# Kernel tuning notes

Measured on AMD Instinct MI355X. Metric: run time of the kernel, lower is better.

Reference implementation:

```python
import jax, jax.numpy as jnp
import numpy as np
from jax import lax

EPS = 1e-5
DIM_1D, DIM_2D, CH, L, B = 788, 210, 64, 384, 1
DILATIONS = (1, 2, 4, 2, 1)


def inorm(x, gamma, beta, axes):
    # InstanceNorm: normalize over spatial axes per (batch, channel), affine params per channel
    mu = jnp.mean(x, axis=axes, keepdims=True)
    var = jnp.mean(jnp.square(x - mu), axis=axes, keepdims=True)
    xn = (x - mu) * lax.rsqrt(var + EPS)
    shape = [1] * x.ndim
    shape[1] = x.shape[1]
    return xn * gamma.reshape(shape) + beta.reshape(shape)


def inorm_noaffine(x, axes):
    mu = jnp.mean(x, axis=axes, keepdims=True)
    var = jnp.mean(jnp.square(x - mu), axis=axes, keepdims=True)
    return (x - mu) * lax.rsqrt(var + EPS)


def conv3x3(x, w, b, d):
    y = lax.conv_general_dilated(x, w, window_strides=(1, 1),
                                 padding=[(d, d), (d, d)], rhs_dilation=(d, d),
                                 dimension_numbers=('NCHW', 'OIHW', 'NCHW'))
    return y + b.reshape(1, -1, 1, 1)


def setup_inputs() -> dict:
    key = jax.random.key(0)
    ks = jax.random.split(key, 16)
    s = 0.02
    inp = {
        'x_1d': jax.random.normal(ks[0], (B, DIM_1D, L), jnp.float32),
        'x_2d': jax.random.normal(ks[1], (B, DIM_2D, L, L), jnp.float32),
        'W1': jax.random.normal(ks[2], (CH, 2 * DIM_1D), jnp.float32) * s,
        'g1': jnp.ones((CH,), jnp.float32), 'b1': jnp.zeros((CH,), jnp.float32),
        'W2': jax.random.normal(ks[3], (CH, DIM_2D), jnp.float32) * s,
        'g2': jnp.ones((CH,), jnp.float32), 'b2': jnp.zeros((CH,), jnp.float32),
        'W3': jax.random.normal(ks[4], (CH, 2 * CH), jnp.float32) * s,
        'g3': jnp.ones((CH,), jnp.float32), 'b3': jnp.zeros((CH,), jnp.float32),
        'res_w': jax.random.normal(ks[5], (5, 2, CH, CH, 3, 3), jnp.float32) * s,
        'res_b': jnp.zeros((5, 2, CH), jnp.float32),
        'res_g': jnp.ones((5, 2, CH), jnp.float32),
        'res_beta': jnp.zeros((5, 2, CH), jnp.float32),
    }
    return inp


def reference(x_1d, x_2d, W1, g1, b1, W2, g2, b2, W3, g3, b3,
              res_w, res_b, res_g, res_beta):
    # pre-norms (no affine)
    x1 = inorm_noaffine(x_1d, axes=(2,))            # [B, D1, L]
    x2 = inorm_noaffine(x_2d, axes=(2, 3))          # [B, D2, L, L]

    # pair_conv1: 1x1 conv on concat(row-expand, col-expand) of x1.
    # Mathematically: W1a @ x1 broadcast over j  +  W1b @ x1 broadcast over i.
    W1a, W1b = W1[:, :DIM_1D], W1[:, DIM_1D:]
    row = jnp.einsum('cd,bdl->bcl', W1a, x1)        # [B, C, L] (row term, index i)
    col = jnp.einsum('cd,bdl->bcl', W1b, x1)        # [B, C, L] (col term, index j)
    pair1 = row[:, :, :, None] + col[:, :, None, :]  # [B, C, L, L]
    pair1 = jax.nn.leaky_relu(inorm(pair1, g1, b1, axes=(2, 3)), 0.01)

    # pair_conv2: 1x1 conv on x2
    pair2 = jnp.einsum('cd,bdij->bcij', W2, x2)
    pair2 = jax.nn.leaky_relu(inorm(pair2, g2, b2, axes=(2, 3)), 0.01)

    # pair_conv3: 1x1 conv on concat([pair1, pair2]) -> split weight, sum
    W3a, W3b = W3[:, :CH], W3[:, CH:]
    pair = jnp.einsum('cd,bdij->bcij', W3a, pair1) + jnp.einsum('cd,bdij->bcij', W3b, pair2)
    x = jax.nn.leaky_relu(inorm(pair, g3, b3, axes=(2, 3)), 0.01)

    # ResNet: 5 blocks, each (conv-IN-lrelu) x2 + residual, dropout=0
    for layer in range(5):
        d = DILATIONS[layer]
        res = x
        for k in range(2):
            x = conv3x3(x, res_w[layer, k], res_b[layer, k], d)
            x = jax.nn.leaky_relu(inorm(x, res_g[layer, k], res_beta[layer, k], axes=(2, 3)), 0.01)
        x = x + res
    return x
```

## Files before the change

kernel.cpp:

```cpp
#include <hip/hip_runtime.h>
#include <hip/hip_bf16.h>

typedef __attribute__((ext_vector_type(8)))  short short8;
typedef __attribute__((ext_vector_type(16))) float floatx16;
typedef unsigned short ushort;

constexpr int SL  = 384;
constexpr int N2  = SL * SL;
constexpr int CH  = 64;
constexpr int D1  = 788;
constexpr int D2  = 210;
constexpr int KG2 = 14;
constexpr float EPSF = 1e-5f;

constexpr int TX = 32, TY = 8;
constexpr int NBLK = (SL / TX) * (SL / TY);


__device__ __forceinline__ float lrelu(float v){ return v >= 0.f ? v : 0.01f * v; }
__device__ __forceinline__ ushort f2b(float f){
  __hip_bfloat16 h = __float2bfloat16(f); return *(ushort*)&h;
}
__device__ __forceinline__ float b2f(ushort u){
  __hip_bfloat16 h = *(__hip_bfloat16*)&u; return __bfloat162float(h);
}

__device__ __forceinline__ float wred(float v){
  #pragma unroll
  for (int o = 32; o; o >>= 1) v += __shfl_down(v, o, 64);
  return v;
}

__global__ void stats_k(const float* __restrict__ x, int n, float* __restrict__ part){
  const int c = blockIdx.y, s = blockIdx.x, S = gridDim.x;
  const int chunk = (n + S - 1) / S;
  const int st = s * chunk, en = min(n, st + chunk);
  const float* p = x + (size_t)c * n;
  float sm = 0.f, ss = 0.f;
  for (int i = st + threadIdx.x; i < en; i += blockDim.x){
    float v = p[i]; sm += v; ss += v * v;
  }
  sm = wred(sm); ss = wred(ss);
  __shared__ float aux[8];
  const int wid = threadIdx.x >> 6, lane = threadIdx.x & 63;
  if (lane == 0){ aux[wid] = sm; aux[4 + wid] = ss; }
  __syncthreads();
  if (threadIdx.x == 0){
    part[((size_t)c * S + s) * 2]     = aux[0] + aux[1] + aux[2] + aux[3];
    part[((size_t)c * S + s) * 2 + 1] = aux[4] + aux[5] + aux[6] + aux[7];
  }
}

__global__ void stats_final_k(const float* __restrict__ part, int C, int S, float ninv,
                              float* __restrict__ mean, float* __restrict__ rstd){
  const int c = blockIdx.x * 64 + (threadIdx.x >> 4);
  const int t = threadIdx.x & 15;
  if (c >= C) return;
  float sm = 0.f, ss = 0.f;
  for (int s = t; s < S; s += 16){
    sm += part[((size_t)c * S + s) * 2];
    ss += part[((size_t)c * S + s) * 2 + 1];
  }
  #pragma unroll
  for (int o = 8; o; o >>= 1){ sm += __shfl_down(sm, o, 16); ss += __shfl_down(ss, o, 16); }
  if (t == 0){
    const float m = sm * ninv;
    mean[c] = m;
    rstd[c] = rsqrtf(ss * ninv - m * m + EPSF);
  }
}

__global__ void statsaffine_k(const float* __restrict__ part, int S, float ninv,
                              const float* __restrict__ g, const float* __restrict__ be,
                              int goff, float* __restrict__ ao, float* __restrict__ bo){
  const int c = threadIdx.x >> 4;
  const int t = threadIdx.x & 15;
  float sm = 0.f, ss = 0.f;
  for (int s = t; s < S; s += 16){
    sm += part[((size_t)c * S + s) * 2];
    ss += part[((size_t)c * S + s) * 2 + 1];
  }
  #pragma unroll
  for (int o = 8; o; o >>= 1){ sm += __shfl_down(sm, o, 16); ss += __shfl_down(ss, o, 16); }
  if (t == 0){
    const float m = sm * ninv;
    const float r = rsqrtf(ss * ninv - m * m + EPSF);
    const float a = r * g[goff + c];
    ao[c] = a;
    bo[c] = be[goff + c] - m * a;
  }
}

__global__ void rowcol_k(const float* __restrict__ x1d, const float* __restrict__ W1,
                         const float* __restrict__ r1, float* __restrict__ rcP){
  const int idx = blockIdx.x * 256 + threadIdx.x;
  const int chunk = blockIdx.y;
  const int half = idx / (CH * SL);
  const int rem  = idx % (CH * SL);
  const int c = rem / SL, l = rem % SL;
  const int d0 = chunk * 197, d1 = min(D1, d0 + 197);
  const float* wp = W1 + (size_t)c * (2 * D1) + (size_t)half * D1;
  float acc = 0.f;
  for (int d = d0; d < d1; ++d)
    acc += wp[d] * (x1d[(size_t)d * SL + l] * r1[d]);
  rcP[(size_t)chunk * (2 * CH * SL) + idx] = acc;
}

__global__ void rowcol_stats_k(const float* __restrict__ rcP,
                               float* __restrict__ m1, float* __restrict__ rs1){
  const int c = blockIdx.x;
  float sr = 0, ssr = 0, sc = 0, ssc = 0;
  for (int i = threadIdx.x; i < SL; i += blockDim.x){
    float r = 0, q = 0;
    #pragma unroll
    for (int k = 0; k < 4; ++k){
      r += rcP[(size_t)k * (2*CH*SL) + c * SL + i];
      q += rcP[(size_t)k * (2*CH*SL) + CH*SL + c * SL + i];
    }
    sr += r; ssr += r * r; sc += q; ssc += q * q;
  }
  sr = wred(sr); ssr = wred(ssr); sc = wred(sc); ssc = wred(ssc);
  __shared__ float aux[16];
  const int wid = threadIdx.x >> 6, lane = threadIdx.x & 63;
  if (lane == 0){ aux[wid] = sr; aux[4+wid] = ssr; aux[8+wid] = sc; aux[12+wid] = ssc; }
  __syncthreads();
  if (threadIdx.x == 0){
    float a = 0, b = 0, d = 0, e = 0;
    for (int i = 0; i < 4; ++i){ a += aux[i]; b += aux[4+i]; d += aux[8+i]; e += aux[12+i]; }
    const float mr = a / SL, mc = d / SL;
    const float vr = b / SL - mr * mr, vc = e / SL - mc * mc;
    m1[c]  = mr + mc;
    rs1[c] = rsqrtf(vr + vc + EPSF);
  }
}

__global__ void rowcolT_k(const float* __restrict__ rcP,
                          const float* __restrict__ m1, const float* __restrict__ rs1,
                          const float* __restrict__ g1, const float* __restrict__ b1,
                          float* __restrict__ rowT, float* __restrict__ colT){
  const int i = blockIdx.x * 256 + threadIdx.x;
  const int l = i >> 6, c = i & 63;
  float r = 0, q = 0;
  #pragma unroll
  for (int k = 0; k < 4; ++k){
    r += rcP[(size_t)k * (2*CH*SL) + c * SL + l];
    q += rcP[(size_t)k * (2*CH*SL) + CH*SL + c * SL + l];
  }
  const float a  = rs1[c] * g1[c];
  const float bb = b1[c] - m1[c] * a;
  rowT[i] = r * a + bb;
  colT[i] = q * a;
}

__global__ __launch_bounds__(256) void pair1n_k(const float* __restrict__ rowT,
                                                const float* __restrict__ colT,
                                                ushort* __restrict__ out){
  const size_t q = ((size_t)blockIdx.x * 256 + threadIdx.x) * 16;
  const int R = (int)(q >> 4);
  const int x = R % SL;
  const int t = R / SL;
  const int kc = t & 3, y = t >> 2;
  const int c0 = kc * 16;
  const float4* rp = (const float4*)&rowT[y * 64 + c0];
  const float4* cp = (const float4*)&colT[x * 64 + c0];
  ushort o[16];
  #pragma unroll
  for (int k = 0; k < 4; ++k){
    float4 r = rp[k], cl = cp[k];
    o[4*k]   = f2b(lrelu(r.x + cl.x));
    o[4*k+1] = f2b(lrelu(r.y + cl.y));
    o[4*k+2] = f2b(lrelu(r.z + cl.z));
    o[4*k+3] = f2b(lrelu(r.w + cl.w));
  }
  *(short8*)&out[q]     = *(short8*)&o[0];
  *(short8*)&out[q + 8] = *(short8*)&o[8];
}

__global__ __launch_bounds__(256) void x2cvt_k(const float* __restrict__ x2,
                                               ushort* __restrict__ x2b,
                                               float* __restrict__ part){
  const int g  = blockIdx.y;
  const int p  = blockIdx.x * 256 + threadIdx.x;
  const int tid = threadIdx.x;
  float v[16];
  #pragma unroll
  for (int i = 0; i < 16; ++i){
    const int d = g * 16 + i;
    v[i] = (d < D2) ? x2[(size_t)d * N2 + p] : 0.f;
  }
  ushort o[16];
  #pragma unroll
  for (int i = 0; i < 16; ++i) o[i] = f2b(v[i]);
  ushort* dp = &x2b[((size_t)g * N2 + p) * 16];
  *(short8*)&dp[0] = *(short8*)&o[0];
  *(short8*)&dp[8] = *(short8*)&o[8];
  __shared__ float aux[4][16][2];
  const int wid = tid >> 6, lane = tid & 63;
  #pragma unroll
  for (int i = 0; i < 16; ++i){
    float a = wred(v[i]), b = wred(v[i] * v[i]);
    if (lane == 0){ aux[wid][i][0] = a; aux[wid][i][1] = b; }
  }
  __syncthreads();
  if (tid < 16){
    const int d = g * 16 + tid;
    if (d < D2){
      float a = aux[0][tid][0] + aux[1][tid][0] + aux[2][tid][0] + aux[3][tid][0];
      float b = aux[0][tid][1] + aux[1][tid][1] + aux[2][tid][1] + aux[3][tid][1];
      part[((size_t)d * gridDim.x + blockIdx.x) * 2]     = a;
      part[((size_t)d * gridDim.x + blockIdx.x) * 2 + 1] = b;
    }
  }
}

__global__ void w2b_k(const float* __restrict__ W2, const float* __restrict__ r2,
                      ushort* __restrict__ w2b){
  const int i = blockIdx.x * 256 + threadIdx.x;
  const int j    = i & 7;
  const int oc   = (i >> 3) & 63;
  const int half = (i >> 9) & 1;
  const int kc   = i >> 10;
  const int d    = kc * 16 + half * 8 + j;
  w2b[i] = (d < D2) ? f2b(W2[(size_t)oc * D2 + d] * r2[d]) : (ushort)0;
}

__global__ __launch_bounds__(256) void pair2m_k(const ushort* __restrict__ x2b,
                                                const ushort* __restrict__ w2b,
                                                ushort* __restrict__ out,
                                                float* __restrict__ part){
  __shared__ __align__(16) unsigned char ldsraw[256 * 144 + 4 * CH * 2 * 4];
  const int tid = threadIdx.x, lane = tid & 63, wid = tid >> 6;
  const int ln = lane & 31, half = lane >> 5;
  const int px0 = blockIdx.x * 256;
  floatx16 acc[2][2];
  #pragma unroll
  for (int mt = 0; mt < 2; ++mt)
    #pragma unroll
    for (int nt = 0; nt < 2; ++nt)
      #pragma unroll
      for (int r = 0; r < 16; ++r) acc[mt][nt][r] = 0.f;

  const int p0w = px0 + wid * 64 + ln;
  #pragma unroll
  for (int kc = 0; kc < KG2; ++kc){
    const ushort* ab = w2b + ((size_t)(kc * 2 + half)) * 512;
    short8 a0 = *(const short8*)&ab[ln * 8];
    short8 a1 = *(const short8*)&ab[256 + ln * 8];
    short8 b0 = *(const short8*)&x2b[((size_t)kc * N2 + p0w) * 16 + half * 8];
    short8 b1 = *(const short8*)&x2b[((size_t)kc * N2 + p0w + 32) * 16 + half * 8];
    acc[0][0] = __builtin_amdgcn_mfma_f32_32x32x16_bf16(a0, b0, acc[0][0], 0, 0, 0);
    acc[1][0] = __builtin_amdgcn_mfma_f32_32x32x16_bf16(a1, b0, acc[1][0], 0, 0, 0);
    acc[0][1] = __builtin_amdgcn_mfma_f32_32x32x16_bf16(a0, b1, acc[0][1], 0, 0, 0);
    acc[1][1] = __builtin_amdgcn_mfma_f32_32x32x16_bf16(a1, b1, acc[1][1], 0, 0, 0);
  }

  ushort* tb = (ushort*)ldsraw;
  float*  sc = (float*)(ldsraw + 256 * 144);
  #pragma unroll
  for (int mt = 0; mt < 2; ++mt)
    #pragma unroll
    for (int nt = 0; nt < 2; ++nt){
      const int pxl = (2*wid + nt) * 32 + ln;
      #pragma unroll
      for (int rq = 0; rq < 4; ++rq){
        const int oc0 = mt*32 + 8*rq + 4*half;
        #pragma unroll
        for (int k = 0; k < 2; ++k){
          const int r = rq*4 + k*2;
          unsigned pk = (unsigned)f2b(acc[mt][nt][r]) | ((unsigned)f2b(acc[mt][nt][r+1]) << 16);
          *(unsigned*)&tb[pxl * 72 + oc0 + k*2] = pk;
        }
      }
    }
  #pragma unroll
  for (int mt = 0; mt < 2; ++mt)
    #pragma unroll
    for (int rq = 0; rq < 4; ++rq)
      #pragma unroll
      for (int t = 0; t < 4; ++t){
        const int r = rq*4 + t;
        float v  = acc[mt][0][r] + acc[mt][1][r];
        float v2 = acc[mt][0][r]*acc[mt][0][r] + acc[mt][1][r]*acc[mt][1][r];
        #pragma unroll
        for (int o = 1; o < 32; o <<= 1){ v += __shfl_xor(v, o, 64); v2 += __shfl_xor(v2, o, 64); }
        if (ln == 0){
          const int oc = mt*32 + 8*rq + 4*half + t;
          sc[(wid*CH + oc)*2] = v; sc[(wid*CH + oc)*2 + 1] = v2;
        }
      }
  __syncthreads();
  {
    const int px = lane & 31, h2 = lane >> 5;
    #pragma unroll
    for (int nt = 0; nt < 2; ++nt){
      const int rr = 2*wid + nt;
      const int p = px0 + rr*32 + px;
      const int y = p / SL, x = p - y * SL;
      #pragma unroll
      for (int h = 0; h < 2; ++h){
        const int kc = h2*2 + h;
        const ushort* sp = &tb[(rr*32 + px) * 72 + kc*16];
        ushort* dp = &out[((size_t)((y*4 + kc) * SL) + x) * 16];
        *(short8*)&dp[0] = *(const short8*)&sp[0];
        *(short8*)&dp[8] = *(const short8*)&sp[8];
      }
    }
  }
  if (tid < CH){
    float sm = 0.f, ss = 0.f;
    #pragma unroll
    for (int w = 0; w < 4; ++w){ sm += sc[(w*CH + tid)*2]; ss += sc[(w*CH + tid)*2 + 1]; }
    part[((size_t)tid * NBLK + blockIdx.x) * 2]     = sm;
    part[((size_t)tid * NBLK + blockIdx.x) * 2 + 1] = ss;
  }
}

__global__ __launch_bounds__(256) void norm_nhwc_k(ushort* __restrict__ x,
                                                   const float* __restrict__ a,
                                                   const float* __restrict__ b){
  const size_t q = ((size_t)blockIdx.x * 256 + threadIdx.x) * 16;
  const int R = (int)(q >> 4);
  const int c0 = ((R / SL) & 3) * 16;
  short8 v0 = *(short8*)&x[q], v1 = *(short8*)&x[q + 8];
  ushort o[16];
  #pragma unroll
  for (int k = 0; k < 8; ++k){
    o[k]   = f2b(lrelu(b2f((ushort)v0[k]) * a[c0+k]   + b[c0+k]));
    o[k+8] = f2b(lrelu(b2f((ushort)v1[k]) * a[c0+8+k] + b[c0+8+k]));
  }
  *(short8*)&x[q]     = *(short8*)&o[0];
  *(short8*)&x[q + 8] = *(short8*)&o[8];
}

__global__ void w3b_k(const float* __restrict__ W3, ushort* __restrict__ w3b){
  const int i = blockIdx.x * 256 + threadIdx.x;
  const int j    = i & 7;
  const int oc   = (i >> 3) & 63;
  const int half = (i >> 9) & 1;
  const int kc   = i >> 10;
  const int e    = kc * 16 + half * 8 + j;
  w3b[i] = f2b(W3[oc * (2 * CH) + e]);
}

__global__ __launch_bounds__(256) void mixm_k(const ushort* __restrict__ A,
                                              const ushort* __restrict__ Bv,
                                              const ushort* __restrict__ w3b,
                                              ushort* __restrict__ out,
                                              float* __restrict__ part){
  __shared__ __align__(16) unsigned char ldsraw[256 * 144 + 4 * CH * 2 * 4];
  const int tid = threadIdx.x, lane = tid & 63, wid = tid >> 6;
  const int ln = lane & 31, half = lane >> 5;
  const int px0 = blockIdx.x * 256;
  floatx16 acc[2][2];
  #pragma unroll
  for (int mt = 0; mt < 2; ++mt)
    #pragma unroll
    for (int nt = 0; nt < 2; ++nt)
      #pragma unroll
      for (int r = 0; r < 16; ++r) acc[mt][nt][r] = 0.f;

  const int p0w = px0 + wid * 64 + ln;
  const int p1w = p0w + 32;
  const int y0 = p0w / SL, x0 = p0w - y0 * SL;
  const int y1 = p1w / SL, x1 = p1w - y1 * SL;
  #pragma unroll
  for (int kc = 0; kc < 8; ++kc){
    const ushort* src = (kc < 4) ? A : Bv;
    const int kcm = kc & 3;
    const ushort* ab = w3b + ((size_t)(kc * 2 + half)) * 512;
    short8 a0 = *(const short8*)&ab[ln * 8];
    short8 a1 = *(const short8*)&ab[256 + ln * 8];
    const size_t r0 = ((size_t)((y0 * 4 + kcm) * SL) + x0) * 16 + half * 8;
    const size_t r1 = ((size_t)((y1 * 4 + kcm) * SL) + x1) * 16 + half * 8;
    short8 b0 = *(const short8*)&src[r0];
    short8 b1 = *(const short8*)&src[r1];
    acc[0][0] = __builtin_amdgcn_mfma_f32_32x32x16_bf16(a0, b0, acc[0][0], 0, 0, 0);
    acc[1][0] = __builtin_amdgcn_mfma_f32_32x32x16_bf16(a1, b0, acc[1][0], 0, 0, 0);
    acc[0][1] = __builtin_amdgcn_mfma_f32_32x32x16_bf16(a0, b1, acc[0][1], 0, 0, 0);
    acc[1][1] = __builtin_amdgcn_mfma_f32_32x32x16_bf16(a1, b1, acc[1][1], 0, 0, 0);
  }

  ushort* tb = (ushort*)ldsraw;
  float*  sc = (float*)(ldsraw + 256 * 144);
  #pragma unroll
  for (int mt = 0; mt < 2; ++mt)
    #pragma unroll
    for (int nt = 0; nt < 2; ++nt){
      const int pxl = (2*wid + nt) * 32 + ln;
      #pragma unroll
      for (int rq = 0; rq < 4; ++rq){
        const int oc0 = mt*32 + 8*rq + 4*half;
        #pragma unroll
        for (int k = 0; k < 2; ++k){
          const int r = rq*4 + k*2;
          unsigned pk = (unsigned)f2b(acc[mt][nt][r]) | ((unsigned)f2b(acc[mt][nt][r+1]) << 16);
          *(unsigned*)&tb[pxl * 72 + oc0 + k*2] = pk;
        }
      }
    }
  #pragma unroll
  for (int mt = 0; mt < 2; ++mt)
    #pragma unroll
    for (int rq = 0; rq < 4; ++rq)
      #pragma unroll
      for (int t = 0; t < 4; ++t){
        const int r = rq*4 + t;
        float v  = acc[mt][0][r] + acc[mt][1][r];
        float v2 = acc[mt][0][r]*acc[mt][0][r] + acc[mt][1][r]*acc[mt][1][r];
        #pragma unroll
        for (int o = 1; o < 32; o <<= 1){ v += __shfl_xor(v, o, 64); v2 += __shfl_xor(v2, o, 64); }
        if (ln == 0){
          const int oc = mt*32 + 8*rq + 4*half + t;
          sc[(wid*CH + oc)*2] = v; sc[(wid*CH + oc)*2 + 1] = v2;
        }
      }
  __syncthreads();
  {
    const int px = lane & 31, h2 = lane >> 5;
    #pragma unroll
    for (int nt = 0; nt < 2; ++nt){
      const int rr = 2*wid + nt;
      const int p = px0 + rr*32 + px;
      const int y = p / SL, x = p - y * SL;
      #pragma unroll
      for (int h = 0; h < 2; ++h){
        const int kc = h2*2 + h;
        const ushort* sp = &tb[(rr*32 + px) * 72 + kc*16];
        ushort* dp = &out[((size_t)((y*4 + kc) * SL) + x) * 16];
        *(short8*)&dp[0] = *(const short8*)&sp[0];
        *(short8*)&dp[8] = *(const short8*)&sp[8];
      }
    }
  }
  if (tid < CH){
    float sm = 0.f, ss = 0.f;
    #pragma unroll
    for (int w = 0; w < 4; ++w){ sm += sc[(w*CH + tid)*2]; ss += sc[(w*CH + tid)*2 + 1]; }
    part[((size_t)tid * NBLK + blockIdx.x) * 2]     = sm;
    part[((size_t)tid * NBLK + blockIdx.x) * 2 + 1] = ss;
  }
}

__global__ __launch_bounds__(256) void norm_res_k(const ushort* __restrict__ src,
                                                  const float* __restrict__ a,
                                                  const float* __restrict__ b,
                                                  float* __restrict__ X,
                                                  ushort* __restrict__ Xb,
                                                  int doRes){
  __shared__ float tf[64 * 68];
  const int tid = threadIdx.x;
  const int p0 = blockIdx.x * 64;
  const int y0 = p0 / SL, x0 = p0 - y0 * SL;
  const int pxl = tid >> 2, kc = tid & 3, c0 = kc * 16;
  {
    const ushort* sp = &src[((size_t)((y0*4 + kc) * SL) + x0 + pxl) * 16];
    short8 v0 = *(const short8*)&sp[0], v1 = *(const short8*)&sp[8];
    #pragma unroll
    for (int k = 0; k < 8; ++k){
      tf[(c0+k)*68 + pxl]   = lrelu(b2f((ushort)v0[k]) * a[c0+k]   + b[c0+k]);
      tf[(c0+8+k)*68 + pxl] = lrelu(b2f((ushort)v1[k]) * a[c0+8+k] + b[c0+8+k]);
    }
  }
  __syncthreads();
  {
    const int c = tid >> 2, part = tid & 3;
    const size_t gb = (size_t)c * N2 + p0 + part * 16;
    float w[16];
    #pragma unroll
    for (int k = 0; k < 16; ++k) w[k] = tf[c*68 + part*16 + k];
    if (doRes){
      #pragma unroll
      for (int k = 0; k < 16; ++k) w[k] += X[gb + k];
      #pragma unroll
      for (int k = 0; k < 16; ++k) tf[c*68 + part*16 + k] = w[k];
    }
    #pragma unroll
    for (int k = 0; k < 16; ++k) X[gb + k] = w[k];
  }
  if (Xb){
    __syncthreads();
    ushort o[16];
    #pragma unroll
    for (int k = 0; k < 16; ++k) o[k] = f2b(tf[(c0+k)*68 + pxl]);
    ushort* xp = &Xb[((size_t)((y0*4 + kc) * SL) + x0 + pxl) * 16];
    *(short8*)&xp[0] = *(short8*)&o[0];
    *(short8*)&xp[8] = *(short8*)&o[8];
  }
}

__global__ void wt_k(const float* __restrict__ w, ushort* __restrict__ wt){
  const int i = blockIdx.x * 256 + threadIdx.x;
  const int j    = i & 7;
  const int oc   = (i >> 3) & 63;
  const int half = (i >> 9) & 1;
  const int kc   = (i >> 10) & 3;
  const int tap  = (i / 4096) % 9;
  const int cv   = i / 36864;
  const int ic   = kc * 16 + half * 8 + j;
  wt[i] = f2b(w[((size_t)(cv * CH + oc) * CH + ic) * 9 + tap]);
}

template<int DIL, bool FUSE>
__global__ __launch_bounds__(256, 3) void convd_k(const ushort* __restrict__ in,
                                                  const ushort* __restrict__ wg,
                                                  const float* __restrict__ na,
                                                  const float* __restrict__ nb,
                                                  ushort* __restrict__ out,
                                                  float* __restrict__ part){
  constexpr int TH = TY + 2 * DIL;
  constexpr int TW = TX + 2 * DIL;
  constexpr int PHASES = (DIL >= 2) ? 2 : 1;
  constexpr int KCP = 4 / PHASES;
  constexpr int STAGE_B = KCP * TH * TW * 32;
  constexpr int EPI_B = 256 * 144 + 4 * CH * 2 * 4;
  constexpr int LDS_B = STAGE_B > EPI_B ? STAGE_B : EPI_B;
  __shared__ __align__(16) unsigned char ldsraw[LDS_B];

  const int tid = threadIdx.x, lane = tid & 63, wid = tid >> 6;
  const int ln = lane & 31, half = lane >> 5;
  const int bx = blockIdx.x % (SL / TX), by = blockIdx.x / (SL / TX);

  floatx16 acc[2][2];
  #pragma unroll
  for (int mt = 0; mt < 2; ++mt)
    #pragma unroll
    for (int nt = 0; nt < 2; ++nt)
      #pragma unroll
      for (int r = 0; r < 16; ++r) acc[mt][nt][r] = 0.f;

  #pragma unroll
  for (int ph = 0; ph < PHASES; ++ph){
    if (ph) __syncthreads();
    constexpr int PIECES = KCP * TH * TW * 2;
    for (int t = tid; t < PIECES; t += 256){
      const int half_ = t & 1;
      const int idx   = t >> 1;
      const int rx    = idx % TW;
      const int rem   = idx / TW;
      const int ry    = rem % TH;
      const int kcl   = rem / TH;
      const int kc    = ph * KCP + kcl;
      const int gy    = by * TY - DIL + ry;
      const int gx    = bx * TX - DIL + rx;
      const unsigned byteoff = ((unsigned)t * 16) ^ (((rx >> 2) & 1) << 4);
      short8 v = {0,0,0,0,0,0,0,0};
      if ((unsigned)gy < (unsigned)SL && (unsigned)gx < (unsigned)SL){
        v = *(const short8*)&in[(((size_t)(gy * 4 + kc)) * SL + gx) * 16 + half_ * 8];
        if (FUSE){
          const int c0 = kc * 16 + half_ * 8;
          float4 a0 = *(const float4*)&na[c0], a1 = *(const float4*)&na[c0 + 4];
          float4 b0 = *(const float4*)&nb[c0], b1 = *(const float4*)&nb[c0 + 4];
          ushort o[8];
          o[0] = f2b(lrelu(b2f((ushort)v[0]) * a0.x + b0.x));
          o[1] = f2b(lrelu(b2f((ushort)v[1]) * a0.y + b0.y));
          o[2] = f2b(lrelu(b2f((ushort)v[2]) * a0.z + b0.z));
          o[3] = f2b(lrelu(b2f((ushort)v[3]) * a0.w + b0.w));
          o[4] = f2b(lrelu(b2f((ushort)v[4]) * a1.x + b1.x));
          o[5] = f2b(lrelu(b2f((ushort)v[5]) * a1.y + b1.y));
          o[6] = f2b(lrelu(b2f((ushort)v[6]) * a1.z + b1.z));
          o[7] = f2b(lrelu(b2f((ushort)v[7]) * a1.w + b1.w));
          v = *(short8*)o;
        }
      }
      *(short8*)(ldsraw + byteoff) = v;
    }
    __syncthreads();
    #pragma unroll
    for (int tap = 0; tap < 9; ++tap){
      const int dy = (tap / 3 - 1) * DIL, dx = (tap % 3 - 1) * DIL;
      const int ry0 = 2 * wid + dy + DIL;
      const int rx  = ln + dx + DIL;
      const unsigned swz = ((unsigned)((rx >> 2) & 1)) << 4;
      #pragma unroll
      for (int kcl = 0; kcl < KCP; ++kcl){
        const int kc = ph * KCP + kcl;
        const ushort* ab = wg + ((size_t)((tap * 4 + kc) * 2 + half)) * 512;
        short8 a0 = *(const short8*)&ab[ln * 8];
        short8 a1 = *(const short8*)&ab[256 + ln * 8];
        const unsigned bo0 = ((unsigned)((((kcl * TH + ry0) * TW + rx) * 2 + half) * 16)) ^ swz;
        const unsigned bo1 = ((unsigned)((((kcl * TH + ry0 + 1) * TW + rx) * 2 + half) * 16)) ^ swz;
        short8 b0 = *(const short8*)(ldsraw + bo0);
        short8 b1 = *(const short8*)(ldsraw + bo1);
        acc[0][0] = __builtin_amdgcn_mfma_f32_32x32x16_bf16(a0, b0, acc[0][0], 0, 0, 0);
        acc[1][0] = __builtin_amdgcn_mfma_f32_32x32x16_bf16(a1, b0, acc[1][0], 0, 0, 0);
        acc[0][1] = __builtin_amdgcn_mfma_f32_32x32x16_bf16(a0, b1, acc[0][1], 0, 0, 0);
        acc[1][1] = __builtin_amdgcn_mfma_f32_32x32x16_bf16(a1, b1, acc[1][1], 0, 0, 0);
      }
    }
  }

  __syncthreads();
  ushort* tb = (ushort*)ldsraw;
  float*  sc = (float*)(ldsraw + 256 * 144);
  #pragma unroll
  for (int mt = 0; mt < 2; ++mt)
    #pragma unroll
    for (int nt = 0; nt < 2; ++nt){
      const int pxl = (2*wid + nt) * 32 + ln;
      #pragma unroll
      for (int rq = 0; rq < 4; ++rq){
        const int oc0 = mt*32 + 8*rq + 4*half;
        #pragma unroll
        for (int k = 0; k < 2; ++k){
          const int r = rq*4 + k*2;
          unsigned pk = (unsigned)f2b(acc[mt][nt][r]) | ((unsigned)f2b(acc[mt][nt][r+1]) << 16);
          *(unsigned*)&tb[pxl * 72 + oc0 + k*2] = pk;
        }
      }
    }
  #pragma unroll
  for (int mt = 0; mt < 2; ++mt)
    #pragma unroll
    for (int rq = 0; rq < 4; ++rq)
      #pragma unroll
      for (int t = 0; t < 4; ++t){
        const int r = rq*4 + t;
        float v  = acc[mt][0][r] + acc[mt][1][r];
        float v2 = acc[mt][0][r]*acc[mt][0][r] + acc[mt][1][r]*acc[mt][1][r];
        #pragma unroll
        for (int o = 1; o < 32; o <<= 1){ v += __shfl_xor(v, o, 64); v2 += __shfl_xor(v2, o, 64); }
        if (ln == 0){
          const int oc = mt*32 + 8*rq + 4*half + t;
          sc[(wid*CH + oc)*2] = v; sc[(wid*CH + oc)*2 + 1] = v2;
        }
      }
  __syncthreads();
  {
    const int px = lane & 31, h2 = lane >> 5;
    #pragma unroll
    for (int nt = 0; nt < 2; ++nt){
      const int rr = 2*wid + nt;
      const int gy = by*TY + rr;
      #pragma unroll
      for (int h = 0; h < 2; ++h){
        const int kc = h2*2 + h;
        const ushort* sp = &tb[(rr*32 + px) * 72 + kc*16];
        ushort* dp = &out[((size_t)((gy*4 + kc) * SL) + bx*TX + px) * 16];
        *(short8*)&dp[0] = *(const short8*)&sp[0];
        *(short8*)&dp[8] = *(const short8*)&sp[8];
      }
    }
  }
  if (tid < CH){
    float sm = 0.f, ss = 0.f;
    #pragma unroll
    for (int w = 0; w < 4; ++w){ sm += sc[(w*CH + tid)*2]; ss += sc[(w*CH + tid)*2 + 1]; }
    part[((size_t)tid * NBLK + blockIdx.x) * 2]     = sm;
    part[((size_t)tid * NBLK + blockIdx.x) * 2 + 1] = ss;
  }
}

static void launch_conv(int dil, bool fuse, const ushort* src, const ushort* wgl,
                        const float* na, const float* nb,
                        ushort* dst, float* part, hipStream_t s){
  if (fuse){
    switch (dil){
      case 1:  convd_k<1,true><<<NBLK, 256, 0, s>>>(src, wgl, na, nb, dst, part); break;
      case 2:  convd_k<2,true><<<NBLK, 256, 0, s>>>(src, wgl, na, nb, dst, part); break;
      default: convd_k<4,true><<<NBLK, 256, 0, s>>>(src, wgl, na, nb, dst, part); break;
    }
  } else {
    switch (dil){
      case 1:  convd_k<1,false><<<NBLK, 256, 0, s>>>(src, wgl, na, nb, dst, part); break;
      case 2:  convd_k<2,false><<<NBLK, 256, 0, s>>>(src, wgl, na, nb, dst, part); break;
      default: convd_k<4,false><<<NBLK, 256, 0, s>>>(src, wgl, na, nb, dst, part); break;
    }
  }
}

extern "C" void kernel_launch(void* const* d_in, const int* in_sizes, int n_in,
                              void* d_out, int out_size, void* d_ws, size_t ws_size,
                              hipStream_t stream){
  const float* x1d    = (const float*)d_in[0];
  const float* x2     = (const float*)d_in[1];
  const float* W1     = (const float*)d_in[2];
  const float* g1     = (const float*)d_in[3];
  const float* b1     = (const float*)d_in[4];
  const float* W2     = (const float*)d_in[5];
  const float* res_w  = (const float*)d_in[11];
  const float* res_g  = (const float*)d_in[13];
  const float* res_be = (const float*)d_in[14];
  float* X = (float*)d_out;

  unsigned char* wp = (unsigned char*)d_ws;
  ushort* A   = (ushort*)wp; wp += (size_t)N2 * 64 * 2;
  ushort* Bb  = (ushort*)wp; wp += (size_t)N2 * 64 * 2;
  ushort* Xb  = (ushort*)wp; wp += (size_t)N2 * 64 * 2;
  ushort* x2b = (ushort*)wp; wp += (size_t)KG2 * N2 * 16 * 2;
  ushort* wt  = (ushort*)wp; wp += (size_t)368640 * 2;
  ushort* w3b = (ushort*)wp; wp += (size_t)8192 * 2;
  ushort* w2b = (ushort*)wp; wp += (size_t)14336 * 2;
  float* fw = (float*)wp;
  float* rcP  = fw; fw += 4 * 2 * CH * SL;
  float* rowT = fw; fw += SL * CH;
  float* colT = fw; fw += SL * CH;
  float* s1m  = fw; fw += D1;   float* s1r = fw; fw += D1;
  float* s2m  = fw; fw += 256;  float* s2r = fw; fw += 256;
  float* m1   = fw; fw += 64;   float* rs1 = fw; fw += 64;
  float* aA   = fw; fw += 64;   float* bA  = fw; fw += 64;
  float* aB   = fw; fw += 64;   float* bB  = fw; fw += 64;
  float* part = fw; fw += (size_t)D2 * NBLK * 2;

  stats_k<<<dim3(1, D1), 256, 0, stream>>>(x1d, SL, part);
  stats_final_k<<<13, 1024, 0, stream>>>(part, D1, 1, 1.f / SL, s1m, s1r);
  rowcol_k<<<dim3(2 * CH * SL / 256, 4), 256, 0, stream>>>(x1d, W1, s1r, rcP);
  rowcol_stats_k<<<CH, 256, 0, stream>>>(rcP, m1, rs1);
  rowcolT_k<<<SL * CH / 256, 256, 0, stream>>>(rcP, m1, rs1, g1, b1, rowT, colT);
  pair1n_k<<<N2 * 64 / 4096, 256, 0, stream>>>(rowT, colT, A);

  x2cvt_k<<<dim3(N2 / 256, KG2), 256, 0, stream>>>(x2, x2b, part);
  stats_final_k<<<4, 1024, 0, stream>>>(part, D2, N2 / 256, 1.f / N2, s2m, s2r);
  w2b_k<<<56, 256, 0, stream>>>(W2, s2r, w2b);
  pair2m_k<<<NBLK, 256, 0, stream>>>(x2b, w2b, Bb, part);
  statsaffine_k<<<1, 1024, 0, stream>>>(part, NBLK, 1.f / N2,
      (const float*)d_in[6], (const float*)d_in[7], 0, aA, bA);
  norm_nhwc_k<<<N2 * 64 / 4096, 256, 0, stream>>>(Bb, aA, bA);

  w3b_k<<<32, 256, 0, stream>>>((const float*)d_in[8], w3b);
  mixm_k<<<NBLK, 256, 0, stream>>>(A, Bb, w3b, A, part);
  statsaffine_k<<<1, 1024, 0, stream>>>(part, NBLK, 1.f / N2,
      (const float*)d_in[9], (const float*)d_in[10], 0, aA, bA);
  norm_res_k<<<N2 / 64, 256, 0, stream>>>(A, aA, bA, X, Xb, 0);

  wt_k<<<368640 / 256, 256, 0, stream>>>(res_w, wt);

  const int dil[5] = {1, 2, 4, 2, 1};
  for (int layer = 0; layer < 5; ++layer){
    const int d = dil[layer];
    const int li0 = layer * 2, li1 = li0 + 1;
    launch_conv(d, false, Xb, wt + (size_t)li0 * 36864, nullptr, nullptr, A, part, stream);
    statsaffine_k<<<1, 1024, 0, stream>>>(part, NBLK, 1.f / N2, res_g, res_be, li0 * CH, aA, bA);
    launch_conv(d, true, A, wt + (size_t)li1 * 36864, aA, bA, Bb, part, stream);
    statsaffine_k<<<1, 1024, 0, stream>>>(part, NBLK, 1.f / N2, res_g, res_be, li1 * CH, aB, bB);
    norm_res_k<<<N2 / 64, 256, 0, stream>>>(Bb, aB, bB, X,
        (layer == 4) ? nullptr : Xb, 1);
  }
}
```

Measured before the change: 1.007 ms.

## Coarsen x2 conversion per block and drop LDS-staged conv epilogue for occupancy

```diff
diff --git a/kernel.cpp b/kernel.cpp
--- a/kernel.cpp
+++ b/kernel.cpp
@@ -15,6 +15,7 @@
 
 constexpr int TX = 32, TY = 8;
 constexpr int NBLK = (SL / TX) * (SL / TY);
+constexpr int XCHUNK = 72;
 
 
 __device__ __forceinline__ float lrelu(float v){ return v >= 0.f ? v : 0.01f * v; }
@@ -176,39 +177,54 @@
   *(short8*)&out[q + 8] = *(short8*)&o[8];
 }
 
-__global__ __launch_bounds__(256) void x2cvt_k(const float* __restrict__ x2,
-                                               ushort* __restrict__ x2b,
-                                               float* __restrict__ part){
-  const int g  = blockIdx.y;
-  const int p  = blockIdx.x * 256 + threadIdx.x;
+__global__ __launch_bounds__(256, 2) void x2cvt_k(const float* __restrict__ x2,
+                                                  ushort* __restrict__ x2b,
+                                                  float* __restrict__ part){
+  const int g   = blockIdx.y;
   const int tid = threadIdx.x;
-  float v[16];
-  #pragma unroll
-  for (int i = 0; i < 16; ++i){
-    const int d = g * 16 + i;
-    v[i] = (d < D2) ? x2[(size_t)d * N2 + p] : 0.f;
-  }
-  ushort o[16];
-  #pragma unroll
-  for (int i = 0; i < 16; ++i) o[i] = f2b(v[i]);
-  ushort* dp = &x2b[((size_t)g * N2 + p) * 16];
-  *(short8*)&dp[0] = *(short8*)&o[0];
-  *(short8*)&dp[8] = *(short8*)&o[8];
+  const int d0  = g * 16;
+  float sm[16], ss[16];
+  #pragma unroll
+  for (int i = 0; i < 16; ++i){ sm[i] = 0.f; ss[i] = 0.f; }
+  #pragma unroll
+  for (int it = 0; it < 4; ++it){
+    const int p = blockIdx.x * 2048 + it * 512 + tid * 2;
+    float2 v[16];
+    #pragma unroll
+    for (int i = 0; i < 16; ++i){
+      const int d = d0 + i;
+      if (d < D2) v[i] = *(const float2*)&x2[(size_t)d * N2 + p];
+      else        v[i] = make_float2(0.f, 0.f);
+    }
+    ushort o[32];
+    #pragma unroll
+    for (int i = 0; i < 16; ++i){
+      o[i]      = f2b(v[i].x);
+      o[16 + i] = f2b(v[i].y);
+      sm[i] += v[i].x + v[i].y;
+      ss[i] += v[i].x * v[i].x + v[i].y * v[i].y;
+    }
+    ushort* dp = &x2b[((size_t)g * N2 + p) * 16];
+    *(short8*)&dp[0]  = *(short8*)&o[0];
+    *(short8*)&dp[8]  = *(short8*)&o[8];
+    *(short8*)&dp[16] = *(short8*)&o[16];
+    *(short8*)&dp[24] = *(short8*)&o[24];
+  }
   __shared__ float aux[4][16][2];
   const int wid = tid >> 6, lane = tid & 63;
   #pragma unroll
   for (int i = 0; i < 16; ++i){
-    float a = wred(v[i]), b = wred(v[i] * v[i]);
+    float a = wred(sm[i]), b = wred(ss[i]);
     if (lane == 0){ aux[wid][i][0] = a; aux[wid][i][1] = b; }
   }
   __syncthreads();
   if (tid < 16){
-    const int d = g * 16 + tid;
+    const int d = d0 + tid;
     if (d < D2){
       float a = aux[0][tid][0] + aux[1][tid][0] + aux[2][tid][0] + aux[3][tid][0];
       float b = aux[0][tid][1] + aux[1][tid][1] + aux[2][tid][1] + aux[3][tid][1];
-      part[((size_t)d * gridDim.x + blockIdx.x) * 2]     = a;
-      part[((size_t)d * gridDim.x + blockIdx.x) * 2 + 1] = b;
+      part[((size_t)d * XCHUNK + blockIdx.x) * 2]     = a;
+      part[((size_t)d * XCHUNK + blockIdx.x) * 2 + 1] = b;
     }
   }
 }
@@ -501,7 +517,7 @@
 }
 
 template<int DIL, bool FUSE>
-__global__ __launch_bounds__(256, 3) void convd_k(const ushort* __restrict__ in,
+__global__ __launch_bounds__(256, 4) void convd_k(const ushort* __restrict__ in,
                                                   const ushort* __restrict__ wg,
                                                   const float* __restrict__ na,
                                                   const float* __restrict__ nb,
@@ -509,12 +525,10 @@
                                                   float* __restrict__ part){
   constexpr int TH = TY + 2 * DIL;
   constexpr int TW = TX + 2 * DIL;
-  constexpr int PHASES = (DIL >= 2) ? 2 : 1;
-  constexpr int KCP = 4 / PHASES;
-  constexpr int STAGE_B = KCP * TH * TW * 32;
-  constexpr int EPI_B = 256 * 144 + 4 * CH * 2 * 4;
-  constexpr int LDS_B = STAGE_B > EPI_B ? STAGE_B : EPI_B;
-  __shared__ __align__(16) unsigned char ldsraw[LDS_B];
+  constexpr int KCP = 2;
+  constexpr int PHASES = 2;
+  __shared__ __align__(16) unsigned char ldsraw[KCP * TH * TW * 32];
+  __shared__ float sc[4 * CH * 2];
 
   const int tid = threadIdx.x, lane = tid & 63, wid = tid >> 6;
   const int ln = lane & 31, half = lane >> 5;
@@ -589,25 +603,25 @@
     }
   }
 
-  __syncthreads();
-  ushort* tb = (ushort*)ldsraw;
-  float*  sc = (float*)(ldsraw + 256 * 144);
-  #pragma unroll
-  for (int mt = 0; mt < 2; ++mt)
+  {
+    const int gx = bx * TX + ln;
     #pragma unroll
     for (int nt = 0; nt < 2; ++nt){
-      const int pxl = (2*wid + nt) * 32 + ln;
-      #pragma unroll
-      for (int rq = 0; rq < 4; ++rq){
-        const int oc0 = mt*32 + 8*rq + 4*half;
+      const int gy = by * TY + 2 * wid + nt;
+      #pragma unroll
+      for (int mt = 0; mt < 2; ++mt)
         #pragma unroll
-        for (int k = 0; k < 2; ++k){
-          const int r = rq*4 + k*2;
-          unsigned pk = (unsigned)f2b(acc[mt][nt][r]) | ((unsigned)f2b(acc[mt][nt][r+1]) << 16);
-          *(unsigned*)&tb[pxl * 72 + oc0 + k*2] = pk;
+        for (int rq = 0; rq < 4; ++rq){
+          const int oc0 = mt * 32 + 8 * rq + 4 * half;
+          const int kc = oc0 >> 4, off = oc0 & 15;
+          const int r = rq * 4;
+          uint2 pk;
+          pk.x = (unsigned)f2b(acc[mt][nt][r])     | ((unsigned)f2b(acc[mt][nt][r+1]) << 16);
+          pk.y = (unsigned)f2b(acc[mt][nt][r+2])   | ((unsigned)f2b(acc[mt][nt][r+3]) << 16);
+          *(uint2*)&out[((size_t)(gy * 4 + kc) * SL + gx) * 16 + off] = pk;
         }
-      }
-    }
+    }
+  }
   #pragma unroll
   for (int mt = 0; mt < 2; ++mt)
     #pragma unroll
@@ -625,22 +639,6 @@
         }
       }
   __syncthreads();
-  {
-    const int px = lane & 31, h2 = lane >> 5;
-    #pragma unroll
-    for (int nt = 0; nt < 2; ++nt){
-      const int rr = 2*wid + nt;
-      const int gy = by*TY + rr;
-      #pragma unroll
-      for (int h = 0; h < 2; ++h){
-        const int kc = h2*2 + h;
-        const ushort* sp = &tb[(rr*32 + px) * 72 + kc*16];
-        ushort* dp = &out[((size_t)((gy*4 + kc) * SL) + bx*TX + px) * 16];
-        *(short8*)&dp[0] = *(const short8*)&sp[0];
-        *(short8*)&dp[8] = *(const short8*)&sp[8];
-      }
-    }
-  }
   if (tid < CH){
     float sm = 0.f, ss = 0.f;
     #pragma unroll
@@ -708,8 +706,8 @@
   rowcolT_k<<<SL * CH / 256, 256, 0, stream>>>(rcP, m1, rs1, g1, b1, rowT, colT);
   pair1n_k<<<N2 * 64 / 4096, 256, 0, stream>>>(rowT, colT, A);
 
-  x2cvt_k<<<dim3(N2 / 256, KG2), 256, 0, stream>>>(x2, x2b, part);
-  stats_final_k<<<4, 1024, 0, stream>>>(part, D2, N2 / 256, 1.f / N2, s2m, s2r);
+  x2cvt_k<<<dim3(XCHUNK, KG2), 256, 0, stream>>>(x2, x2b, part);
+  stats_final_k<<<4, 1024, 0, stream>>>(part, D2, XCHUNK, 1.f / N2, s2m, s2r);
   w2b_k<<<56, 256, 0, stream>>>(W2, s2r, w2b);
   pair2m_k<<<NBLK, 256, 0, stream>>>(x2b, w2b, Bb, part);
   statsaffine_k<<<1, 1024, 0, stream>>>(part, NBLK, 1.f / N2,
```

Measured after the change: 1.006 ms. Within noise of the previous version (-0.1%).
